# Performance work log

Measured on AMD Instinct MI355X. Metric: run time of the kernel, lower is better.

## Reference

```python
import jax, jax.numpy as jnp
import numpy as np

N1, N2, C = 1024, 1024, 128
H = 2 * C  # h_dim = in_dim * 2


def setup_inputs() -> dict:
    key = jax.random.key(0)
    ks = jax.random.split(key, 8)
    std = 0.01
    return {
        "X": jax.random.normal(ks[0], (N1, C), dtype=jnp.float32),
        "Y": jax.random.normal(ks[1], (N2, C), dtype=jnp.float32),
        "Wsr": jax.random.normal(ks[2], (C, C), dtype=jnp.float32) * std,
        "Wtg": jax.random.normal(ks[3], (C, C), dtype=jnp.float32) * std,
        "W1": jax.random.normal(ks[4], (H, H), dtype=jnp.float32) * std,
        "b1": jnp.zeros((H,), dtype=jnp.float32),
        "W2": jax.random.normal(ks[5], (1, H), dtype=jnp.float32) * std,
        "b2": jnp.zeros((1,), dtype=jnp.float32),
    }


def reference(X, Y, Wsr, Wtg, W1, b1, W2, b2):
    # project_sr / project_tg (bias-free Linear: x @ W^T)
    Xp = X @ Wsr.T  # [N1, C]
    Yp = Y @ Wtg.T  # [N2, C]
    # First fc_M linear on concat([X_k, Y_k]) == split-weight form:
    # concat(x, y) @ W1^T = x @ W1[:, :C]^T + y @ W1[:, C:]^T
    Xh = Xp @ W1[:, :C].T  # [N1, 2C]
    Yh = Yp @ W1[:, C:].T  # [N2, 2C]
    Hid = jax.nn.relu(Xh[:, None, :] + Yh[None, :, :] + b1)  # [N1, N2, 2C]
    # Second linear 2C -> 1, then squeeze
    M = jnp.einsum('abh,h->ab', Hid, W2[0]) + b2[0]  # [N1, N2]
    return M
```

## Files before the change

### kernel.cpp

```cpp
#include <hip/hip_runtime.h>

#define N1 1024
#define N2 1024
#define CDIM 128
#define HDIM 256


__global__ __launch_bounds__(256) void fold_weights(
    const float* __restrict__ W1, const float* __restrict__ Wsr,
    const float* __restrict__ Wtg, float* __restrict__ Wx,
    float* __restrict__ Wy) {
  int id = blockIdx.x * 256 + threadIdx.x;
  int m  = id / (HDIM * CDIM);
  int r  = id % (HDIM * CDIM);
  int h  = r / CDIM;
  int j  = r % CDIM;
  const float* Wm    = m ? Wtg : Wsr;
  const float* w1row = W1 + (size_t)h * HDIM + (m ? CDIM : 0);
  float acc = 0.f;
#pragma unroll 8
  for (int c = 0; c < CDIM; ++c)
    acc = fmaf(w1row[c], Wm[(size_t)c * CDIM + j], acc);
  (m ? Wy : Wx)[(size_t)h * CDIM + j] = acc;
}

__global__ __launch_bounds__(256) void gemm_ht(
    const float* __restrict__ X, const float* __restrict__ Y,
    const float* __restrict__ Wx, const float* __restrict__ Wy,
    const float* __restrict__ b1, float* __restrict__ XhT,
    float* __restrict__ YhT) {
  const float* A = blockIdx.z ? Y : X;
  const float* W = blockIdx.z ? Wy : Wx;
  float*       O = blockIdx.z ? YhT : XhT;
  const bool useBias = (blockIdx.z == 0);

  __shared__ float Al[64][132];
  __shared__ float Wl[128][68];

  const int t  = threadIdx.x;
  const int n0 = blockIdx.x * 64;
  const int h0 = blockIdx.y * 64;

#pragma unroll
  for (int it = 0; it < 8; ++it) {
    int row = it * 8 + (t >> 5);
    int col = (t & 31) * 4;
    *(float4*)(&Al[row][col]) =
        *(const float4*)(&A[(size_t)(n0 + row) * CDIM + col]);
  }
#pragma unroll
  for (int it = 0; it < 8; ++it) {
    int h = it * 8 + (t >> 5);
    int k = (t & 31) * 4;
    float4 w = *(const float4*)(&W[(size_t)(h0 + h) * CDIM + k]);
    Wl[k + 0][h] = w.x;
    Wl[k + 1][h] = w.y;
    Wl[k + 2][h] = w.z;
    Wl[k + 3][h] = w.w;
  }
  __syncthreads();

  const int tx = t & 15;
  const int ty = t >> 4;
  float acc[4][4];
#pragma unroll
  for (int i = 0; i < 4; ++i)
#pragma unroll
    for (int j = 0; j < 4; ++j) acc[i][j] = 0.f;

  for (int k4 = 0; k4 < CDIM; k4 += 4) {
    float a_[4][4];
#pragma unroll
    for (int i = 0; i < 4; ++i) {
      float4 v = *(const float4*)(&Al[ty * 4 + i][k4]);
      a_[i][0] = v.x; a_[i][1] = v.y; a_[i][2] = v.z; a_[i][3] = v.w;
    }
#pragma unroll
    for (int kk = 0; kk < 4; ++kk) {
      float4 w = *(const float4*)(&Wl[k4 + kk][tx * 4]);
      float wj[4] = {w.x, w.y, w.z, w.w};
#pragma unroll
      for (int i = 0; i < 4; ++i)
#pragma unroll
        for (int j = 0; j < 4; ++j)
          acc[i][j] = fmaf(a_[i][kk], wj[j], acc[i][j]);
    }
  }

#pragma unroll
  for (int j = 0; j < 4; ++j) {
    int h = h0 + tx * 4 + j;
    float b = useBias ? b1[h] : 0.f;
    float4 v = {acc[0][j] + b, acc[1][j] + b, acc[2][j] + b, acc[3][j] + b};
    *(float4*)(&O[(size_t)h * N1 + n0 + ty * 4]) = v;
  }
}

__global__ __launch_bounds__(256) void pairwise(
    const float* __restrict__ XhT, const float* __restrict__ YhT,
    const float* __restrict__ W2, const float* __restrict__ b2,
    float* __restrict__ M) {
  __shared__ float Xl[64][64];
  __shared__ float Yl[64][64];

  const int t  = threadIdx.x;
  const int tx = t & 15;
  const int ty = t >> 4;
  const int b0 = blockIdx.x * 64;
  const int a0 = blockIdx.y * 64;

  float acc[4][4];
#pragma unroll
  for (int i = 0; i < 4; ++i)
#pragma unroll
    for (int j = 0; j < 4; ++j) acc[i][j] = 0.f;

  for (int hc = 0; hc < HDIM; hc += 64) {
#pragma unroll
    for (int it = 0; it < 4; ++it) {
      int hl = it * 16 + (t >> 4);
      int c4 = (t & 15) * 4;
      *(float4*)(&Xl[hl][c4]) =
          *(const float4*)(&XhT[(size_t)(hc + hl) * N1 + a0 + c4]);
      *(float4*)(&Yl[hl][c4]) =
          *(const float4*)(&YhT[(size_t)(hc + hl) * N2 + b0 + c4]);
    }
    __syncthreads();

    for (int h4 = 0; h4 < 64; h4 += 4) {
      float4 w4 = *(const float4*)(&W2[hc + h4]);
      float wh[4] = {w4.x, w4.y, w4.z, w4.w};
#pragma unroll
      for (int hh = 0; hh < 4; ++hh) {
        int h = h4 + hh;
        float4 xv = *(const float4*)(&Xl[h][ty * 4]);
        float4 yv = *(const float4*)(&Yl[h][tx * 4]);
        float xa[4] = {xv.x, xv.y, xv.z, xv.w};
        float yb[4] = {yv.x, yv.y, yv.z, yv.w};
#pragma unroll
        for (int i = 0; i < 4; ++i)
#pragma unroll
          for (int j = 0; j < 4; ++j) {
            float s = xa[i] + yb[j];
            acc[i][j] = fmaf(fmaxf(s, 0.f), wh[hh], acc[i][j]);
          }
      }
    }
    __syncthreads();
  }

  const float bb = b2[0];
#pragma unroll
  for (int i = 0; i < 4; ++i) {
    int a = a0 + ty * 4 + i;
    float4 v = {acc[i][0] + bb, acc[i][1] + bb, acc[i][2] + bb,
                acc[i][3] + bb};
    *(float4*)(&M[(size_t)a * N2 + b0 + tx * 4]) = v;
  }
}

extern "C" void kernel_launch(void* const* d_in, const int* in_sizes, int n_in,
                              void* d_out, int out_size, void* d_ws,
                              size_t ws_size, hipStream_t stream) {
  const float* X   = (const float*)d_in[0];
  const float* Y   = (const float*)d_in[1];
  const float* Wsr = (const float*)d_in[2];
  const float* Wtg = (const float*)d_in[3];
  const float* W1  = (const float*)d_in[4];
  const float* b1  = (const float*)d_in[5];
  const float* W2  = (const float*)d_in[6];
  const float* b2  = (const float*)d_in[7];
  float* out = (float*)d_out;

  float* ws  = (float*)d_ws;
  float* Wx  = ws;
  float* Wy  = ws + 32768;
  float* XhT = ws + 65536;
  float* YhT = ws + 65536 + 262144;

  fold_weights<<<256, 256, 0, stream>>>(W1, Wsr, Wtg, Wx, Wy);
  gemm_ht<<<dim3(16, 4, 2), 256, 0, stream>>>(X, Y, Wx, Wy, b1, XhT, YhT);
  pairwise<<<dim3(16, 16), 256, 0, stream>>>(XhT, YhT, W2, b2, out);
}
```

Measured before the change: 117.2 us.

## Split pairwise hidden-dim reduction across blocks with partial sums and finalize kernel

The pairwise kernel now splits the 256-wide hidden reduction into four 64-wide chunks along grid z, giving 1024 blocks instead of 256 so the device is better filled. Each block writes a partial [N1,N2] sum to workspace, and a new finalize kernel adds the four partials plus the bias. In exchange it writes and reads 16 MB of extra partial buffers and adds a kernel launch.

```diff
diff --git a/kernel.cpp b/kernel.cpp
--- a/kernel.cpp
+++ b/kernel.cpp
@@ -96,18 +96,32 @@
   }
 }
 
-__global__ __launch_bounds__(256) void pairwise(
+__global__ __launch_bounds__(256, 4) void pairwise_half(
     const float* __restrict__ XhT, const float* __restrict__ YhT,
-    const float* __restrict__ W2, const float* __restrict__ b2,
-    float* __restrict__ M) {
+    const float* __restrict__ W2, float* __restrict__ Pbase) {
   __shared__ float Xl[64][64];
   __shared__ float Yl[64][64];
 
   const int t  = threadIdx.x;
+  const int b0 = blockIdx.x * 64;
+  const int a0 = blockIdx.y * 64;
+  const int hb = blockIdx.z * 64;
+  float* P = Pbase + (size_t)blockIdx.z * ((size_t)N1 * N2);
+
+#pragma unroll
+  for (int it = 0; it < 4; ++it) {
+    int idx = it * 256 + t;
+    int hl  = idx >> 4;
+    int c4  = (idx & 15) * 4;
+    *(float4*)(&Xl[hl][c4]) =
+        *(const float4*)(&XhT[(size_t)(hb + hl) * N1 + a0 + c4]);
+    *(float4*)(&Yl[hl][c4]) =
+        *(const float4*)(&YhT[(size_t)(hb + hl) * N2 + b0 + c4]);
+  }
+  __syncthreads();
+
   const int tx = t & 15;
   const int ty = t >> 4;
-  const int b0 = blockIdx.x * 64;
-  const int a0 = blockIdx.y * 64;
 
   float acc[4][4];
 #pragma unroll
@@ -115,48 +129,47 @@
 #pragma unroll
     for (int j = 0; j < 4; ++j) acc[i][j] = 0.f;
 
-  for (int hc = 0; hc < HDIM; hc += 64) {
-#pragma unroll
-    for (int it = 0; it < 4; ++it) {
-      int hl = it * 16 + (t >> 4);
-      int c4 = (t & 15) * 4;
-      *(float4*)(&Xl[hl][c4]) =
-          *(const float4*)(&XhT[(size_t)(hc + hl) * N1 + a0 + c4]);
-      *(float4*)(&Yl[hl][c4]) =
-          *(const float4*)(&YhT[(size_t)(hc + hl) * N2 + b0 + c4]);
+#pragma unroll 2
+  for (int h4 = 0; h4 < 64; h4 += 4) {
+    float4 w4 = *(const float4*)(&W2[hb + h4]);
+    float wh[4] = {w4.x, w4.y, w4.z, w4.w};
+#pragma unroll
+    for (int hh = 0; hh < 4; ++hh) {
+      float4 xv = *(const float4*)(&Xl[h4 + hh][ty * 4]);
+      float4 yv = *(const float4*)(&Yl[h4 + hh][tx * 4]);
+      float xa[4] = {xv.x, xv.y, xv.z, xv.w};
+      float yb[4] = {yv.x, yv.y, yv.z, yv.w};
+#pragma unroll
+      for (int i = 0; i < 4; ++i)
+#pragma unroll
+        for (int j = 0; j < 4; ++j) {
+          float s = xa[i] + yb[j];
+          acc[i][j] = fmaf(fmaxf(s, 0.f), wh[hh], acc[i][j]);
+        }
     }
-    __syncthreads();
-
-    for (int h4 = 0; h4 < 64; h4 += 4) {
-      float4 w4 = *(const float4*)(&W2[hc + h4]);
-      float wh[4] = {w4.x, w4.y, w4.z, w4.w};
-#pragma unroll
-      for (int hh = 0; hh < 4; ++hh) {
-        int h = h4 + hh;
-        float4 xv = *(const float4*)(&Xl[h][ty * 4]);
-        float4 yv = *(const float4*)(&Yl[h][tx * 4]);
-        float xa[4] = {xv.x, xv.y, xv.z, xv.w};
-        float yb[4] = {yv.x, yv.y, yv.z, yv.w};
-#pragma unroll
-        for (int i = 0; i < 4; ++i)
-#pragma unroll
-          for (int j = 0; j < 4; ++j) {
-            float s = xa[i] + yb[j];
-            acc[i][j] = fmaf(fmaxf(s, 0.f), wh[hh], acc[i][j]);
-          }
-      }
-    }
-    __syncthreads();
-  }
-
-  const float bb = b2[0];
+  }
+
 #pragma unroll
   for (int i = 0; i < 4; ++i) {
     int a = a0 + ty * 4 + i;
-    float4 v = {acc[i][0] + bb, acc[i][1] + bb, acc[i][2] + bb,
-                acc[i][3] + bb};
-    *(float4*)(&M[(size_t)a * N2 + b0 + tx * 4]) = v;
-  }
+    float4 v = {acc[i][0], acc[i][1], acc[i][2], acc[i][3]};
+    *(float4*)(&P[(size_t)a * N2 + b0 + tx * 4]) = v;
+  }
+}
+
+__global__ __launch_bounds__(256) void finalize(
+    const float* __restrict__ P0, const float* __restrict__ P1,
+    const float* __restrict__ P2, const float* __restrict__ P3,
+    const float* __restrict__ b2, float* __restrict__ out) {
+  int i4 = blockIdx.x * 256 + threadIdx.x;
+  float4 a = ((const float4*)P0)[i4];
+  float4 b = ((const float4*)P1)[i4];
+  float4 c = ((const float4*)P2)[i4];
+  float4 d = ((const float4*)P3)[i4];
+  const float bb = b2[0];
+  float4 o = {a.x + b.x + c.x + d.x + bb, a.y + b.y + c.y + d.y + bb,
+              a.z + b.z + c.z + d.z + bb, a.w + b.w + c.w + d.w + bb};
+  ((float4*)out)[i4] = o;
 }
 
 extern "C" void kernel_launch(void* const* d_in, const int* in_sizes, int n_in,
@@ -177,8 +190,11 @@
   float* Wy  = ws + 32768;
   float* XhT = ws + 65536;
   float* YhT = ws + 65536 + 262144;
+  float* P   = ws + 589824;
 
   fold_weights<<<256, 256, 0, stream>>>(W1, Wsr, Wtg, Wx, Wy);
   gemm_ht<<<dim3(16, 4, 2), 256, 0, stream>>>(X, Y, Wx, Wy, b1, XhT, YhT);
-  pairwise<<<dim3(16, 16), 256, 0, stream>>>(XhT, YhT, W2, b2, out);
-}
+  pairwise_half<<<dim3(16, 16, 4), 256, 0, stream>>>(XhT, YhT, W2, P);
+  finalize<<<1024, 256, 0, stream>>>(P, P + 1048576, P + 2097152,
+                                     P + 3145728, b2, out);
+}
```

New measurement: 112.2 us. 1.05x faster.
